# Kernel optimization log

Hardware: AMD Instinct MI355X
Metric: run time of the kernel (lower is better)

Reference implementation:

```python
import jax, jax.numpy as jnp
import numpy as np

TEMPERATURE = 0.07
MASK_VAL = -65504.0  # torch code's fill value (fp16 min), note: applied BEFORE temperature division
EPS = 1e-8


def setup_inputs() -> dict:
    key = jax.random.key(0)
    z = jax.random.normal(key, (8192, 1024), dtype=jnp.float32)
    return {"z": z}


def reference(z):
    N = z.shape[0]
    # cosine similarity via normalized GEMM (torch clamps norm at eps)
    norms = jnp.maximum(jnp.linalg.norm(z, axis=-1, keepdims=True), EPS)
    zn = z / norms
    cos_sim = zn @ zn.T  # [N, N]
    eye = jnp.eye(N, dtype=bool)
    cos_sim = jnp.where(eye, MASK_VAL, cos_sim) / TEMPERATURE
    # pos_mask = eye rolled by N//2 along dim 0 -> pos_mask[i, (i - N//2) % N] = True
    idx = jnp.arange(N)
    pos = cos_sim[idx, (idx - N // 2) % N]
    nll = -pos + jax.nn.logsumexp(cos_sim, axis=-1)
    return nll.mean()
```

## Files before the change

### kernel.cpp

```cpp
#include <hip/hip_runtime.h>
#include <hip/hip_bf16.h>


#define N 8192
#define D 1024
#define INV_T 14.285714285714286f

typedef __bf16 bf16x8 __attribute__((ext_vector_type(8)));
typedef float f32x4 __attribute__((ext_vector_type(4)));

__device__ inline void gload16(const void* g, void* l) {
  __builtin_amdgcn_global_load_lds(
      (const __attribute__((address_space(1))) void*)g,
      (__attribute__((address_space(3))) void*)l, 16, 0, 0);
}

__device__ inline unsigned short f32_to_bf16(float f) {
  unsigned int u = __float_as_uint(f);
  unsigned int r = (u + 0x7FFFu + ((u >> 16) & 1u)) >> 16;
  return (unsigned short)r;
}

__global__ __launch_bounds__(256) void k_normalize(const float* __restrict__ z,
                                                   unsigned short* __restrict__ zn) {
  const int row = blockIdx.x;
  const int t = threadIdx.x;
  const float4 v = ((const float4*)(z + (size_t)row * D))[t];
  float ss = v.x * v.x + v.y * v.y + v.z * v.z + v.w * v.w;
#pragma unroll
  for (int off = 32; off > 0; off >>= 1) ss += __shfl_down(ss, off, 64);
  __shared__ float red[4];
  __shared__ float s_inv;
  if ((t & 63) == 0) red[t >> 6] = ss;
  __syncthreads();
  if (t == 0) {
    float tot = red[0] + red[1] + red[2] + red[3];
    s_inv = 1.0f / fmaxf(sqrtf(tot), 1e-8f);
  }
  __syncthreads();
  const float inv = s_inv;
  ushort4 o;
  o.x = f32_to_bf16(v.x * inv);
  o.y = f32_to_bf16(v.y * inv);
  o.z = f32_to_bf16(v.z * inv);
  o.w = f32_to_bf16(v.w * inv);
  ((ushort4*)(zn + (size_t)row * D))[t] = o;
}

__global__ __launch_bounds__(512, 2) void k_tile(const unsigned short* __restrict__ zn,
                                                 float* __restrict__ rowsum,
                                                 float* __restrict__ pos) {
  __shared__ __align__(16) char smem[65536];
  const int tid = threadIdx.x;
  const int w = tid >> 6, l = tid & 63;

  const int b = blockIdx.x;
  int tr = (int)((sqrtf(8.0f * (float)b + 1.0f) - 1.0f) * 0.5f);
  if (tr * (tr + 1) / 2 > b) --tr;
  if ((tr + 1) * (tr + 2) / 2 <= b) ++tr;
  const int tc = b - tr * (tr + 1) / 2;
  const bool diag = (tr == tc);

  const int wr = w >> 1, wc = w & 1;
  const int m = l & 15, kg = l >> 4;
  const int rowA0 = tr * 256, colB0 = tc * 256;

  f32x4 acc[4][8] = {};

  const int s0 = tid, s1 = 512 + tid;

  {
    const char* base = (const char*)zn;
    char* ab = smem;
    gload16(base + ((size_t)(rowA0 + (s0 >> 2)) * 2048 + (s0 & 3) * 16), ab + s0 * 16);
    gload16(base + ((size_t)(rowA0 + (s1 >> 2)) * 2048 + (s1 & 3) * 16), ab + s1 * 16);
    if (!diag) {
      char* bb = smem + 16384;
      gload16(base + ((size_t)(colB0 + (s0 >> 2)) * 2048 + (s0 & 3) * 16), bb + s0 * 16);
      gload16(base + ((size_t)(colB0 + (s1 >> 2)) * 2048 + (s1 & 3) * 16), bb + s1 * 16);
    }
  }
  __syncthreads();

  for (int kt = 0; kt < 32; ++kt) {
    const int p = kt & 1;
    if (kt < 31) {
      const size_t kb = (size_t)(kt + 1) * 64;
      char* ab = smem + (p ^ 1) * 32768;
      gload16((const char*)zn + ((size_t)(rowA0 + (s0 >> 2)) * 2048 + kb + (s0 & 3) * 16), ab + s0 * 16);
      gload16((const char*)zn + ((size_t)(rowA0 + (s1 >> 2)) * 2048 + kb + (s1 & 3) * 16), ab + s1 * 16);
      if (!diag) {
        char* bb = ab + 16384;
        gload16((const char*)zn + ((size_t)(colB0 + (s0 >> 2)) * 2048 + kb + (s0 & 3) * 16), bb + s0 * 16);
        gload16((const char*)zn + ((size_t)(colB0 + (s1 >> 2)) * 2048 + kb + (s1 & 3) * 16), bb + s1 * 16);
      }
    }
    const char* ab = smem + p * 32768;
    const char* bb = diag ? ab : (ab + 16384);
    bf16x8 af[4], bfr[8];
#pragma unroll
    for (int mt = 0; mt < 4; ++mt)
      af[mt] = *(const bf16x8*)(ab + (wr * 64 + mt * 16 + m) * 64 + kg * 16);
#pragma unroll
    for (int nt = 0; nt < 8; ++nt)
      bfr[nt] = *(const bf16x8*)(bb + (wc * 128 + nt * 16 + m) * 64 + kg * 16);
#pragma unroll
    for (int mt = 0; mt < 4; ++mt)
#pragma unroll
      for (int nt = 0; nt < 8; ++nt)
        acc[mt][nt] = __builtin_amdgcn_mfma_f32_16x16x32_bf16(af[mt], bfr[nt], acc[mt][nt], 0, 0, 0);
    __syncthreads();
  }

  const int quad = l >> 4;
  const int col = l & 15;
  float cs[8] = {0.f, 0.f, 0.f, 0.f, 0.f, 0.f, 0.f, 0.f};
#pragma unroll
  for (int mt = 0; mt < 4; ++mt) {
    float rs[4] = {0.f, 0.f, 0.f, 0.f};
#pragma unroll
    for (int nt = 0; nt < 8; ++nt) {
      const int gcol = colB0 + wc * 128 + nt * 16 + col;
#pragma unroll
      for (int r = 0; r < 4; ++r) {
        const int grow = rowA0 + wr * 64 + mt * 16 + quad * 4 + r;
        const float t = acc[mt][nt][r] * INV_T;
        if (gcol == (grow ^ (N / 2))) {
          pos[grow] = t;
          pos[gcol] = t;
        }
        const float e = (gcol == grow) ? 0.0f : __expf(t - INV_T);
        rs[r] += e;
        cs[nt] += e;
      }
    }
#pragma unroll
    for (int off = 1; off < 16; off <<= 1) {
#pragma unroll
      for (int r = 0; r < 4; ++r) rs[r] += __shfl_xor(rs[r], off, 64);
    }
    if (col == 0) {
#pragma unroll
      for (int r = 0; r < 4; ++r)
        atomicAdd(&rowsum[rowA0 + wr * 64 + mt * 16 + quad * 4 + r], rs[r]);
    }
  }
  if (!diag) {
#pragma unroll
    for (int nt = 0; nt < 8; ++nt) {
      cs[nt] += __shfl_xor(cs[nt], 16, 64);
      cs[nt] += __shfl_xor(cs[nt], 32, 64);
    }
    if (l < 16) {
#pragma unroll
      for (int nt = 0; nt < 8; ++nt)
        atomicAdd(&rowsum[colB0 + wc * 128 + nt * 16 + l], cs[nt]);
    }
  }
}

__global__ __launch_bounds__(256) void k_final(const float* __restrict__ rowsum,
                                               const float* __restrict__ pos,
                                               float* __restrict__ out) {
  const int t = threadIdx.x;
  const int i = blockIdx.x * 256 + t;
  float s = INV_T + __logf(rowsum[i]) - pos[i];
#pragma unroll
  for (int off = 32; off > 0; off >>= 1) s += __shfl_down(s, off, 64);
  __shared__ float red[4];
  if ((t & 63) == 0) red[t >> 6] = s;
  __syncthreads();
  if (t == 0) atomicAdd(out, (red[0] + red[1] + red[2] + red[3]) * (1.0f / N));
}

extern "C" void kernel_launch(void* const* d_in, const int* in_sizes, int n_in,
                              void* d_out, int out_size, void* d_ws, size_t ws_size,
                              hipStream_t stream) {
  const float* z = (const float*)d_in[0];
  float* out = (float*)d_out;
  char* ws = (char*)d_ws;
  unsigned short* zn = (unsigned short*)ws;
  float* rowsum = (float*)(ws + (size_t)N * D * 2);
  float* pos = (float*)(ws + (size_t)N * D * 2 + (size_t)N * 4);

  hipMemsetAsync(rowsum, 0, (size_t)N * sizeof(float), stream);
  hipMemsetAsync(out, 0, sizeof(float), stream);
  k_normalize<<<N, 256, 0, stream>>>(z, zn);
  const int ntiles = (N / 256) * (N / 256 + 1) / 2;
  k_tile<<<ntiles, 512, 0, stream>>>(zn, rowsum, pos);
  k_final<<<N / 256, 256, 0, stream>>>(rowsum, pos, out);
}
```

Before: 175.1 us.

## Double K-tile depth with XOR-swizzled LDS, fold memsets into kernels

The GEMM tile kernel now stages 128-wide K slices instead of 64, using 128 KB of dynamic LDS split into two buffers. The LDS layout uses an XOR swizzle on 16-byte chunks to avoid bank conflicts on fragment reads. This halves the number of barrier-separated iterations, but at 128 KB per block only one block fits per CU, which conflicts with the launch bound's two-block occupancy hint. The two memsets are folded into the normalize kernel and a single-block final reduction that writes the output directly, removing launches and atomics.

```diff
diff --git a/kernel.cpp b/kernel.cpp
--- a/kernel.cpp
+++ b/kernel.cpp
@@ -22,9 +22,11 @@
 }
 
 __global__ __launch_bounds__(256) void k_normalize(const float* __restrict__ z,
-                                                   unsigned short* __restrict__ zn) {
+                                                   unsigned short* __restrict__ zn,
+                                                   float* __restrict__ rowsum) {
   const int row = blockIdx.x;
   const int t = threadIdx.x;
+  if (row < 32) rowsum[row * 256 + t] = 0.0f;
   const float4 v = ((const float4*)(z + (size_t)row * D))[t];
   float ss = v.x * v.x + v.y * v.y + v.z * v.z + v.w * v.w;
 #pragma unroll
@@ -50,7 +52,7 @@
 __global__ __launch_bounds__(512, 2) void k_tile(const unsigned short* __restrict__ zn,
                                                  float* __restrict__ rowsum,
                                                  float* __restrict__ pos) {
-  __shared__ __align__(16) char smem[65536];
+  extern __shared__ __align__(16) char smem[];
   const int tid = threadIdx.x;
   const int w = tid >> 6, l = tid & 63;
 
@@ -67,48 +69,69 @@
 
   f32x4 acc[4][8] = {};
 
-  const int s0 = tid, s1 = 512 + tid;
+  int srow[4], scol[4];
+#pragma unroll
+  for (int j = 0; j < 4; ++j) {
+    int s = j * 512 + tid;
+    int r = s >> 3;
+    srow[j] = r;
+    scol[j] = (s & 7) ^ (r & 7);
+  }
 
   {
-    const char* base = (const char*)zn;
     char* ab = smem;
-    gload16(base + ((size_t)(rowA0 + (s0 >> 2)) * 2048 + (s0 & 3) * 16), ab + s0 * 16);
-    gload16(base + ((size_t)(rowA0 + (s1 >> 2)) * 2048 + (s1 & 3) * 16), ab + s1 * 16);
+    char* bb = smem + 32768;
+#pragma unroll
+    for (int j = 0; j < 4; ++j) {
+      const int s = j * 512 + tid;
+      gload16((const char*)zn + ((size_t)(rowA0 + srow[j]) * 2048 + scol[j] * 16), ab + s * 16);
+    }
     if (!diag) {
-      char* bb = smem + 16384;
-      gload16(base + ((size_t)(colB0 + (s0 >> 2)) * 2048 + (s0 & 3) * 16), bb + s0 * 16);
-      gload16(base + ((size_t)(colB0 + (s1 >> 2)) * 2048 + (s1 & 3) * 16), bb + s1 * 16);
-    }
-  }
-  __syncthreads();
-
-  for (int kt = 0; kt < 32; ++kt) {
-    const int p = kt & 1;
-    if (kt < 31) {
-      const size_t kb = (size_t)(kt + 1) * 64;
-      char* ab = smem + (p ^ 1) * 32768;
-      gload16((const char*)zn + ((size_t)(rowA0 + (s0 >> 2)) * 2048 + kb + (s0 & 3) * 16), ab + s0 * 16);
-      gload16((const char*)zn + ((size_t)(rowA0 + (s1 >> 2)) * 2048 + kb + (s1 & 3) * 16), ab + s1 * 16);
+#pragma unroll
+      for (int j = 0; j < 4; ++j) {
+        const int s = j * 512 + tid;
+        gload16((const char*)zn + ((size_t)(colB0 + srow[j]) * 2048 + scol[j] * 16), bb + s * 16);
+      }
+    }
+  }
+  __syncthreads();
+
+  for (int kt = 0; kt < 16; ++kt) {
+    if (kt < 15) {
+      const size_t kb = (size_t)(kt + 1) * 128;
+      char* ab = smem + ((kt + 1) & 1) * 65536;
+#pragma unroll
+      for (int j = 0; j < 4; ++j) {
+        const int s = j * 512 + tid;
+        gload16((const char*)zn + ((size_t)(rowA0 + srow[j]) * 2048 + kb + scol[j] * 16), ab + s * 16);
+      }
       if (!diag) {
-        char* bb = ab + 16384;
-        gload16((const char*)zn + ((size_t)(colB0 + (s0 >> 2)) * 2048 + kb + (s0 & 3) * 16), bb + s0 * 16);
-        gload16((const char*)zn + ((size_t)(colB0 + (s1 >> 2)) * 2048 + kb + (s1 & 3) * 16), bb + s1 * 16);
-      }
-    }
-    const char* ab = smem + p * 32768;
-    const char* bb = diag ? ab : (ab + 16384);
-    bf16x8 af[4], bfr[8];
-#pragma unroll
-    for (int mt = 0; mt < 4; ++mt)
-      af[mt] = *(const bf16x8*)(ab + (wr * 64 + mt * 16 + m) * 64 + kg * 16);
-#pragma unroll
-    for (int nt = 0; nt < 8; ++nt)
-      bfr[nt] = *(const bf16x8*)(bb + (wc * 128 + nt * 16 + m) * 64 + kg * 16);
-#pragma unroll
-    for (int mt = 0; mt < 4; ++mt)
+        char* bb = ab + 32768;
+#pragma unroll
+        for (int j = 0; j < 4; ++j) {
+          const int s = j * 512 + tid;
+          gload16((const char*)zn + ((size_t)(colB0 + srow[j]) * 2048 + kb + scol[j] * 16), bb + s * 16);
+        }
+      }
+    }
+    const char* ab = smem + (kt & 1) * 65536;
+    const char* bb = diag ? ab : (ab + 32768);
+#pragma unroll
+    for (int ks = 0; ks < 2; ++ks) {
+      bf16x8 af[4], bfr[8];
+      const int csw = ((ks * 4 + kg) ^ (m & 7)) * 16;
+#pragma unroll
+      for (int mt = 0; mt < 4; ++mt)
+        af[mt] = *(const bf16x8*)(ab + (wr * 64 + mt * 16 + m) * 128 + csw);
 #pragma unroll
       for (int nt = 0; nt < 8; ++nt)
-        acc[mt][nt] = __builtin_amdgcn_mfma_f32_16x16x32_bf16(af[mt], bfr[nt], acc[mt][nt], 0, 0, 0);
+        bfr[nt] = *(const bf16x8*)(bb + (wc * 128 + nt * 16 + m) * 128 + csw);
+#pragma unroll
+      for (int mt = 0; mt < 4; ++mt)
+#pragma unroll
+        for (int nt = 0; nt < 8; ++nt)
+          acc[mt][nt] = __builtin_amdgcn_mfma_f32_16x16x32_bf16(af[mt], bfr[nt], acc[mt][nt], 0, 0, 0);
+    }
     __syncthreads();
   }
 
@@ -163,14 +186,14 @@
                                                const float* __restrict__ pos,
                                                float* __restrict__ out) {
   const int t = threadIdx.x;
-  const int i = blockIdx.x * 256 + t;
-  float s = INV_T + __logf(rowsum[i]) - pos[i];
+  float s = 0.f;
+  for (int i = t; i < N; i += 256) s += INV_T + __logf(rowsum[i]) - pos[i];
 #pragma unroll
   for (int off = 32; off > 0; off >>= 1) s += __shfl_down(s, off, 64);
   __shared__ float red[4];
   if ((t & 63) == 0) red[t >> 6] = s;
   __syncthreads();
-  if (t == 0) atomicAdd(out, (red[0] + red[1] + red[2] + red[3]) * (1.0f / N));
+  if (t == 0) out[0] = (red[0] + red[1] + red[2] + red[3]) * (1.0f / N);
 }
 
 extern "C" void kernel_launch(void* const* d_in, const int* in_sizes, int n_in,
@@ -183,10 +206,15 @@
   float* rowsum = (float*)(ws + (size_t)N * D * 2);
   float* pos = (float*)(ws + (size_t)N * D * 2 + (size_t)N * 4);
 
-  hipMemsetAsync(rowsum, 0, (size_t)N * sizeof(float), stream);
-  hipMemsetAsync(out, 0, sizeof(float), stream);
-  k_normalize<<<N, 256, 0, stream>>>(z, zn);
+  static bool attr_set = false;
+  if (!attr_set) {
+    hipFuncSetAttribute((const void*)k_tile,
+                        hipFuncAttributeMaxDynamicSharedMemorySize, 131072);
+    attr_set = true;
+  }
+
+  k_normalize<<<N, 256, 0, stream>>>(z, zn, rowsum);
   const int ntiles = (N / 256) * (N / 256 + 1) / 2;
-  k_tile<<<ntiles, 512, 0, stream>>>(zn, rowsum, pos);
-  k_final<<<N / 256, 256, 0, stream>>>(rowsum, pos, out);
-}
+  k_tile<<<ntiles, 512, 131072, stream>>>(zn, rowsum, pos);
+  k_final<<<1, 256, 0, stream>>>(rowsum, pos, out);
+}
```

Result: faster. 164.0 us (-6.4%).
